# Performance work log

Hardware: AMD Instinct MI355X
Metric: run time of the kernel (lower is better)

The kernel has to match this reference:

```python
import jax, jax.numpy as jnp
import numpy as np

B, C, U, V, H, W = 4, 64, 5, 5, 64, 64
MID = 64  # mid_dim defaults to dim


def setup_inputs() -> dict:
    key = jax.random.key(0)
    ks = jax.random.split(key, 13)
    s = 0.05
    inp = {"x": jax.random.normal(ks[0], (B, C, U, V, H, W), dtype=jnp.float32)}
    # body: Conv2d(dim->mid,1x1), SiLU, Conv2d(mid->dim,1x1)
    inp["w1"] = jax.random.normal(ks[1], (MID, C), dtype=jnp.float32) * s
    inp["b1"] = jax.random.normal(ks[2], (MID,), dtype=jnp.float32) * s
    inp["w2"] = jax.random.normal(ks[3], (C, MID), dtype=jnp.float32) * s
    inp["b2"] = jax.random.normal(ks[4], (C,), dtype=jnp.float32) * s
    # four fuse 1x1 convs (dim->dim)
    for i in range(4):
        inp[f"fw{i}"] = jax.random.normal(ks[5 + 2 * i], (C, C), dtype=jnp.float32) * s
        inp[f"fb{i}"] = jax.random.normal(ks[6 + 2 * i], (C,), dtype=jnp.float32) * s
    return inp


def _conv1x1(w, b, x):
    # x: (B,C,h,w); w: (O,C); 1x1 conv == channel matmul
    return jnp.einsum('oc,bchw->bohw', w, x) + b[None, :, None, None]


def reference(x, w1, b1, w2, b2, fw0, fb0, fw1, fb1, fw2, fb2, fw3, fb3):
    # Four 2-axis mean pools over the 6D tensor
    hw_m = x.mean(axis=(2, 3))   # (B,C,H,W)
    uv_m = x.mean(axis=(4, 5))   # (B,C,U,V)
    uh_m = x.mean(axis=(3, 5))   # (B,C,U,H)
    vw_m = x.mean(axis=(2, 4))   # (B,C,V,W)
    # Assemble padded buffer uvhw of shape (B,C,H+V,W+U)
    top = jnp.concatenate([hw_m, jnp.swapaxes(uh_m, -1, -2)], axis=-1)  # (B,C,H,W+U)
    bot = jnp.concatenate([vw_m, jnp.swapaxes(uv_m, -1, -2)], axis=-1)  # (B,C,V,W+U)
    uvhw = jnpp_concat = jnp.concatenate([top, bot], axis=-2)           # (B,C,H+V,W+U)
    # body: conv1x1 -> SiLU -> conv1x1
    uvhw = _conv1x1(w2, b2, jax.nn.silu(_conv1x1(w1, b1, uvhw)))
    # Split back into the four pooled maps
    hw = uvhw[..., :H, :W]
    vw = uvhw[..., H:, :W]
    uh = jnp.swapaxes(uvhw[..., :H, W:], -1, -2)  # (B,C,U,H)
    uv = jnp.swapaxes(uvhw[..., H:, W:], -1, -2)  # (B,C,U,V)
    # Per-branch fuse convs, then broadcast-gate x and sum
    hw = _conv1x1(fw0, fb0, hw).reshape(B, C, 1, 1, H, W)
    uv = _conv1x1(fw1, fb1, uv).reshape(B, C, U, V, 1, 1)
    uh = _conv1x1(fw2, fb2, uh).reshape(B, C, U, 1, H, 1)
    vw = _conv1x1(fw3, fb3, vw).reshape(B, C, 1, V, 1, W)
    return x * hw + x * uv + x * uh + x * vw
```

## Files before the change

### kernel.cpp

```cpp
#include <hip/hip_runtime.h>
#include <hip/hip_bf16.h>
#include <cstddef>

#define BB 4
#define CC 64
#define UU 5
#define VV 5
#define HH 64
#define WW 64
#define NIJ (69*69)

typedef float f4v __attribute__((ext_vector_type(4)));

__device__ __forceinline__ float rdlane(float v, int l) {
    return __uint_as_float((unsigned)__builtin_amdgcn_readlane((int)__float_as_uint(v), l));
}
__device__ __forceinline__ float sum4(float4 a) { return (a.x+a.y)+(a.z+a.w); }
__device__ __forceinline__ void nt_store4(float4 r, float4* p) {
    union { float4 s; f4v v; } u; u.s = r;
    __builtin_nontemporal_store(u.v, (f4v*)p);
}

__global__ __launch_bounds__(512) void k1_means(const float* __restrict__ x,
        float* __restrict__ part_hw, float* __restrict__ part_vw,
        float* __restrict__ part_uv) {
    const int blk = blockIdx.x;
    const int bc  = blk / 5;
    const int u   = blk % 5;
    const int b   = bc >> 6;
    const int c   = bc & 63;
    const int pidx = (b*5 + u)*64 + c;
    const float4* xt = (const float4*)x + (size_t)bc * 25600 + (size_t)u * 5120;
    const int t    = threadIdx.x;
    const int wave = t >> 6;
    const int lane = t & 63;

    __shared__ float4 vw_lds[8][5][16];

    float4 A[5], B[5];
    #pragma unroll
    for (int v = 0; v < 5; ++v) {
        A[v] = xt[v*1024 + t];
        B[v] = xt[v*1024 + 512 + t];
    }

    float4 hw0 = make_float4(0.f,0.f,0.f,0.f);
    float4 hw1 = make_float4(0.f,0.f,0.f,0.f);
    float4 cs[5];
    #pragma unroll
    for (int v = 0; v < 5; ++v) {
        float4 a = A[v], d = B[v];
        hw0.x += a.x; hw0.y += a.y; hw0.z += a.z; hw0.w += a.w;
        hw1.x += d.x; hw1.y += d.y; hw1.z += d.z; hw1.w += d.w;
        cs[v].x = a.x + d.x; cs[v].y = a.y + d.y;
        cs[v].z = a.z + d.z; cs[v].w = a.w + d.w;
    }

    float4* ph4 = (float4*)part_hw + (size_t)pidx * 1024;
    ph4[t]       = hw0;
    ph4[512 + t] = hw1;

    #pragma unroll
    for (int v = 0; v < 5; ++v) {
        float4 s = cs[v];
        s.x += __shfl_xor(s.x, 16); s.y += __shfl_xor(s.y, 16);
        s.z += __shfl_xor(s.z, 16); s.w += __shfl_xor(s.w, 16);
        s.x += __shfl_xor(s.x, 32); s.y += __shfl_xor(s.y, 32);
        s.z += __shfl_xor(s.z, 32); s.w += __shfl_xor(s.w, 32);
        if (lane < 16) vw_lds[wave][v][lane] = s;
    }
    __syncthreads();

    if (t < 80) {
        const int v = t >> 4;
        float4 s = vw_lds[0][v][t & 15];
        #pragma unroll
        for (int w8 = 1; w8 < 8; ++w8) {
            float4 p = vw_lds[w8][v][t & 15];
            s.x += p.x; s.y += p.y; s.z += p.z; s.w += p.w;
        }
        ((float4*)part_vw)[(size_t)pidx*80 + t] = s;
        float hs = sum4(s);
        hs += __shfl_xor(hs, 1); hs += __shfl_xor(hs, 2);
        hs += __shfl_xor(hs, 4); hs += __shfl_xor(hs, 8);
        if ((t & 15) == 0)
            part_uv[((size_t)(b*5 + v)*5 + u)*64 + c] = hs;
    }
}

__global__ __launch_bounds__(512) void k1b_assemble(
        const float* __restrict__ part_hw, const float* __restrict__ part_vw,
        const float* __restrict__ part_uv, float* __restrict__ grid_t) {
    __shared__ float tile[64][68];
    const int blk = blockIdx.x;
    const bool top = blk < 256;
    const int t = threadIdx.x;
    const int c = t >> 3;
    const int q = t & 7;

    int b, i;
    if (top) {
        b = blk >> 6;
        const int h = blk & 63;
        i = h;
        float4 acc0 = make_float4(0.f,0.f,0.f,0.f);
        float4 acc1 = make_float4(0.f,0.f,0.f,0.f);
        float uhv[5];
        #pragma unroll
        for (int u = 0; u < 5; ++u) {
            const float4* src = (const float4*)part_hw
                + ((size_t)((b*5 + u)*64 + c)) * 1024 + h*16;
            float4 p0 = src[q];
            float4 p1 = src[8 + q];
            acc0.x += p0.x; acc0.y += p0.y; acc0.z += p0.z; acc0.w += p0.w;
            acc1.x += p1.x; acc1.y += p1.y; acc1.z += p1.z; acc1.w += p1.w;
            float uu = sum4(p0) + sum4(p1);
            uu += __shfl_xor(uu, 1); uu += __shfl_xor(uu, 2); uu += __shfl_xor(uu, 4);
            uhv[u] = uu;
        }
        const float s25 = 1.f/25.f;
        const int w0 = q*4, w1 = 32 + q*4;
        tile[w0+0][c] = acc0.x*s25; tile[w0+1][c] = acc0.y*s25;
        tile[w0+2][c] = acc0.z*s25; tile[w0+3][c] = acc0.w*s25;
        tile[w1+0][c] = acc1.x*s25; tile[w1+1][c] = acc1.y*s25;
        tile[w1+2][c] = acc1.z*s25; tile[w1+3][c] = acc1.w*s25;
        if (q == 0) {
            #pragma unroll
            for (int u = 0; u < 5; ++u)
                grid_t[((size_t)b*NIJ + h*69 + 64 + u)*64 + c] = uhv[u] * (1.f/320.f);
        }
    } else {
        b = (blk - 256) / 5;
        const int v = (blk - 256) % 5;
        i = 64 + v;
        float4 a0 = make_float4(0.f,0.f,0.f,0.f);
        float4 a1 = make_float4(0.f,0.f,0.f,0.f);
        #pragma unroll
        for (int u = 0; u < 5; ++u) {
            const float4* src = (const float4*)part_vw
                + ((size_t)((b*5 + u)*64 + c)) * 80 + v*16;
            float4 p0 = src[q];
            float4 p1 = src[8 + q];
            a0.x += p0.x; a0.y += p0.y; a0.z += p0.z; a0.w += p0.w;
            a1.x += p1.x; a1.y += p1.y; a1.z += p1.z; a1.w += p1.w;
        }
        const float sc = 1.f/320.f;
        const int w0 = q*4, w1 = 32 + q*4;
        tile[w0+0][c] = a0.x*sc; tile[w0+1][c] = a0.y*sc;
        tile[w0+2][c] = a0.z*sc; tile[w0+3][c] = a0.w*sc;
        tile[w1+0][c] = a1.x*sc; tile[w1+1][c] = a1.y*sc;
        tile[w1+2][c] = a1.z*sc; tile[w1+3][c] = a1.w*sc;
        if (t < 320) {
            const int u = t >> 6, cc = t & 63;
            grid_t[((size_t)b*NIJ + i*69 + 64 + u)*64 + cc] =
                part_uv[((size_t)(b*5 + v)*5 + u)*64 + cc] * (1.f/4096.f);
        }
    }
    __syncthreads();

    float4* dst4 = (float4*)grid_t + ((size_t)b*NIJ + i*69) * 16;
    #pragma unroll
    for (int k = 0; k < 2; ++k) {
        const int oidx = k*512 + t;
        const int w = oidx >> 4, cq = (oidx & 15) * 4;
        float4 v;
        v.x = tile[w][cq]; v.y = tile[w][cq+1];
        v.z = tile[w][cq+2]; v.w = tile[w][cq+3];
        dst4[oidx] = v;
    }
}

#define LOADROW(dst, src)                                              \
    { _Pragma("unroll")                                                \
      for (int q = 0; q < 16; ++q) {                                   \
          float4 t4 = ((const float4*)(src))[lane*16 + q];             \
          dst[4*q+0] = t4.x; dst[4*q+1] = t4.y;                        \
          dst[4*q+2] = t4.z; dst[4*q+3] = t4.w;                        \
      } }

#define DOT64(res, wr, src)                                            \
    float res;                                                         \
    { float _a0=0.f,_a1=0.f,_a2=0.f,_a3=0.f;                           \
      _Pragma("unroll")                                                \
      for (int cc2 = 0; cc2 < 64; cc2 += 4) {                          \
          _a0 = fmaf(wr[cc2+0], rdlane(src, cc2+0), _a0);              \
          _a1 = fmaf(wr[cc2+1], rdlane(src, cc2+1), _a1);              \
          _a2 = fmaf(wr[cc2+2], rdlane(src, cc2+2), _a2);              \
          _a3 = fmaf(wr[cc2+3], rdlane(src, cc2+3), _a3);              \
      }                                                                \
      res = (_a0 + _a1) + (_a2 + _a3); }

#define MLP_BODY(J)                                                    \
    {                                                                  \
        const int jj = (J);                                            \
        float v = gtb[(size_t)(i*69 + jj) * CC + lane];                \
        DOT64(d1, w1r, v);                                             \
        float acc1 = d1 + b1v;                                         \
        float ya = acc1 / (1.f + __expf(-acc1));                       \
        DOT64(d2, w2r, ya);                                            \
        float acc2 = d2 + b2v;                                         \
        DOT64(d3, fr, acc2);                                           \
        sp[(size_t)(jj - jbase) * sstr] = d3 + fbv;                    \
    }

__global__ __launch_bounds__(64, 1) void k2_mlp(
        const float* __restrict__ grid_t,
        const float* __restrict__ w1, const float* __restrict__ b1,
        const float* __restrict__ w2, const float* __restrict__ b2,
        const float* __restrict__ fw0, const float* __restrict__ fb0,
        const float* __restrict__ fw1, const float* __restrict__ fb1,
        const float* __restrict__ fw2, const float* __restrict__ fb2,
        const float* __restrict__ fw3, const float* __restrict__ fb3,
        float* __restrict__ mod_hw, float* __restrict__ mod_uh,
        float* __restrict__ mod_vw, float* __restrict__ mod_uv) {
    const int blk  = blockIdx.x;
    const int row  = blk >> 2;
    const int chnk = blk & 3;
    const int b    = row / 69;
    const int i    = row % 69;
    const int lane = threadIdx.x & 63;

    const int j0 = chnk * 18;
    const int j1 = min(69, j0 + 18);
    const bool top = (i < 64);

    const float* fwA = top ? fw0 : fw3;
    const float* fbA = top ? fb0 : fb3;
    const float* fwB = top ? fw2 : fw1;
    const float* fbB = top ? fb2 : fb1;

    float w1r[64], w2r[64], fr[64];
    LOADROW(w1r, w1);
    LOADROW(w2r, w2);
    const float b1v = b1[lane];
    const float b2v = b2[lane];

    const float* gtb = grid_t + (size_t)b * NIJ * CC;
    const int cbl = b * CC + lane;

    const int jm = min(j1, 64);
    if (j0 < jm) {
        LOADROW(fr, fwA);
        const float fbv = fbA[lane];
        float* sp; int sstr; const int jbase = 0;
        if (top) { sp = mod_hw + ((size_t)cbl*64 + i)*64;          sstr = 1; }
        else     { sp = mod_vw + (size_t)cbl*320 + (i-64)*64;      sstr = 1; }
        for (int j = j0; j < jm; ++j) MLP_BODY(j)
    }
    if (j1 > 64) {
        LOADROW(fr, fwB);
        const float fbv = fbB[lane];
        float* sp; int sstr; const int jbase = 64;
        if (top) { sp = mod_uh + (size_t)cbl*320 + i;              sstr = 64; }
        else     { sp = mod_uv + (size_t)cbl*25 + (i-64);          sstr = 5;  }
        const int jb = max(j0, 64);
        for (int j = jb; j < j1; ++j) MLP_BODY(j)
    }
}

__global__ __launch_bounds__(256) void k3_apply(
        const float* __restrict__ x,
        const float* __restrict__ mod_hw, const float* __restrict__ mod_uh,
        const float* __restrict__ mod_vw, const float* __restrict__ mod_uv,
        float* __restrict__ out) {
    const int blk  = blockIdx.x;
    const int bc   = blk >> 2;
    const int qt   = blk & 3;
    const int t    = threadIdx.x;
    const int base = qt*256 + t;
    const int h    = base >> 4;

    float4 mh = ((const float4*)(mod_hw + (size_t)bc * 4096))[base];
    float uh[5];
    #pragma unroll
    for (int u = 0; u < 5; ++u) uh[u] = mod_uh[(size_t)bc*320 + u*64 + h];
    float4 vw[5];
    #pragma unroll
    for (int v = 0; v < 5; ++v)
        vw[v] = ((const float4*)(mod_vw + (size_t)bc*320 + v*64))[t & 15];
    float uv[25];
    #pragma unroll
    for (int k = 0; k < 25; ++k) uv[k] = mod_uv[(size_t)bc*25 + k];

    const float4* x4 = (const float4*)(x + (size_t)bc * (UU*VV*HH*WW));
    float4* o4 = (float4*)(out + (size_t)bc * (UU*VV*HH*WW));

    #pragma unroll
    for (int u = 0; u < 5; ++u) {
        #pragma unroll
        for (int v = 0; v < 5; ++v) {
            const int idx = (u*5 + v)*1024 + base;
            float4 xv = x4[idx];
            const float s = uh[u] + uv[u*5 + v];
            float4 r;
            r.x = xv.x * (mh.x + vw[v].x + s);
            r.y = xv.y * (mh.y + vw[v].y + s);
            r.z = xv.z * (mh.z + vw[v].z + s);
            r.w = xv.w * (mh.w + vw[v].w + s);
            nt_store4(r, &o4[idx]);
        }
    }
}

extern "C" void kernel_launch(void* const* d_in, const int* in_sizes, int n_in,
                              void* d_out, int out_size, void* d_ws, size_t ws_size,
                              hipStream_t stream) {
    const float* x   = (const float*)d_in[0];
    const float* w1  = (const float*)d_in[1];
    const float* b1  = (const float*)d_in[2];
    const float* w2  = (const float*)d_in[3];
    const float* b2  = (const float*)d_in[4];
    const float* fw0 = (const float*)d_in[5];
    const float* fb0 = (const float*)d_in[6];
    const float* fw1 = (const float*)d_in[7];
    const float* fb1 = (const float*)d_in[8];
    const float* fw2 = (const float*)d_in[9];
    const float* fb2 = (const float*)d_in[10];
    const float* fw3 = (const float*)d_in[11];
    const float* fb3 = (const float*)d_in[12];

    float* ws = (float*)d_ws;
    float* grid_t = ws;
    float* mod_hw = ws + 1218816;
    float* mod_uh = mod_hw + 1048576;
    float* mod_vw = mod_uh + 81920;
    float* mod_uv = mod_vw + 81920;

    float* part_hw = (float*)d_out;
    float* part_vw = part_hw + 5242880;
    float* part_uv = part_vw + 409600;

    k1_means<<<BB*CC*UU, 512, 0, stream>>>(x, part_hw, part_vw, part_uv);
    k1b_assemble<<<BB*CC + BB*VV, 512, 0, stream>>>(part_hw, part_vw, part_uv, grid_t);
    k2_mlp<<<BB*69*4, 64, 0, stream>>>(grid_t, w1, b1, w2, b2,
                                       fw0, fb0, fw1, fb1, fw2, fb2, fw3, fb3,
                                       mod_hw, mod_uh, mod_vw, mod_uv);
    k3_apply<<<BB*CC*4, 256, 0, stream>>>(x, mod_hw, mod_uh, mod_vw, mod_uv,
                                          (float*)d_out);
}
```

Baseline: 108.4 us.

## Repartition mean reduction over (b,c,spatial-quarter) to shrink partial buffers

The first pass now assigns each block to one (b,c) and a quarter of the HW plane, looping over all 25 (u,v) slices. This lets it write final hw and uh means directly instead of per-u partials of the full HW plane, which were about 5x larger and had to be re-read by the assemble kernel. vw and uv still go through small per-quarter partials reduced in the assemble kernel. It also adds occupancy hints and readfirstlane for the uv scalars in the apply kernel. In exchange, each thread holds more registers (25 uv accumulators) and makes more cross-lane shuffles.

```diff
diff --git a/kernel.cpp b/kernel.cpp
--- a/kernel.cpp
+++ b/kernel.cpp
@@ -15,153 +15,160 @@
 __device__ __forceinline__ float rdlane(float v, int l) {
     return __uint_as_float((unsigned)__builtin_amdgcn_readlane((int)__float_as_uint(v), l));
 }
+__device__ __forceinline__ float rfl(float v) {
+    return __uint_as_float((unsigned)__builtin_amdgcn_readfirstlane((int)__float_as_uint(v)));
+}
 __device__ __forceinline__ float sum4(float4 a) { return (a.x+a.y)+(a.z+a.w); }
 __device__ __forceinline__ void nt_store4(float4 r, float4* p) {
     union { float4 s; f4v v; } u; u.s = r;
     __builtin_nontemporal_store(u.v, (f4v*)p);
 }
 
-__global__ __launch_bounds__(512) void k1_means(const float* __restrict__ x,
-        float* __restrict__ part_hw, float* __restrict__ part_vw,
-        float* __restrict__ part_uv) {
-    const int blk = blockIdx.x;
-    const int bc  = blk / 5;
-    const int u   = blk % 5;
-    const int b   = bc >> 6;
-    const int c   = bc & 63;
-    const int pidx = (b*5 + u)*64 + c;
-    const float4* xt = (const float4*)x + (size_t)bc * 25600 + (size_t)u * 5120;
-    const int t    = threadIdx.x;
+__global__ __launch_bounds__(256, 4) void k1_means(const float* __restrict__ x,
+        float* __restrict__ m_hw, float* __restrict__ m_uh,
+        float* __restrict__ vw_part, float* __restrict__ uv_part) {
+    const int bid = blockIdx.x;
+    const int bc  = bid >> 2;
+    const int qt  = bid & 3;
+    const int t   = threadIdx.x;
+    const int p   = qt*256 + t;
     const int wave = t >> 6;
     const int lane = t & 63;
 
-    __shared__ float4 vw_lds[8][5][16];
-
-    float4 A[5], B[5];
+    const float4* xt = (const float4*)x + (size_t)bc * 25600;
+
+    __shared__ float4 vw_lds[4][5][16];
+    __shared__ float  uv_lds[4][25];
+
+    float4 hw = make_float4(0.f,0.f,0.f,0.f);
+    float4 vwacc[5];
+    #pragma unroll
+    for (int v = 0; v < 5; ++v) vwacc[v] = make_float4(0.f,0.f,0.f,0.f);
+    float uvacc[25];
+
+    #pragma unroll
+    for (int u = 0; u < 5; ++u) {
+        float uhrow = 0.f;
+        #pragma unroll
+        for (int v = 0; v < 5; ++v) {
+            float4 q = xt[(u*5 + v)*1024 + p];
+            hw.x += q.x; hw.y += q.y; hw.z += q.z; hw.w += q.w;
+            vwacc[v].x += q.x; vwacc[v].y += q.y;
+            vwacc[v].z += q.z; vwacc[v].w += q.w;
+            float s4 = sum4(q);
+            uvacc[u*5 + v] = s4;
+            uhrow += s4;
+        }
+        float r = uhrow;
+        r += __shfl_xor(r, 1); r += __shfl_xor(r, 2);
+        r += __shfl_xor(r, 4); r += __shfl_xor(r, 8);
+        if ((t & 15) == 0)
+            m_uh[(size_t)bc*320 + u*64 + qt*16 + (t >> 4)] = r * (1.f/320.f);
+    }
+
+    float4 o;
+    o.x = hw.x*(1.f/25.f); o.y = hw.y*(1.f/25.f);
+    o.z = hw.z*(1.f/25.f); o.w = hw.w*(1.f/25.f);
+    ((float4*)m_hw)[(size_t)bc*1024 + p] = o;
+
     #pragma unroll
     for (int v = 0; v < 5; ++v) {
-        A[v] = xt[v*1024 + t];
-        B[v] = xt[v*1024 + 512 + t];
-    }
-
-    float4 hw0 = make_float4(0.f,0.f,0.f,0.f);
-    float4 hw1 = make_float4(0.f,0.f,0.f,0.f);
-    float4 cs[5];
-    #pragma unroll
-    for (int v = 0; v < 5; ++v) {
-        float4 a = A[v], d = B[v];
-        hw0.x += a.x; hw0.y += a.y; hw0.z += a.z; hw0.w += a.w;
-        hw1.x += d.x; hw1.y += d.y; hw1.z += d.z; hw1.w += d.w;
-        cs[v].x = a.x + d.x; cs[v].y = a.y + d.y;
-        cs[v].z = a.z + d.z; cs[v].w = a.w + d.w;
-    }
-
-    float4* ph4 = (float4*)part_hw + (size_t)pidx * 1024;
-    ph4[t]       = hw0;
-    ph4[512 + t] = hw1;
-
-    #pragma unroll
-    for (int v = 0; v < 5; ++v) {
-        float4 s = cs[v];
+        float4 s = vwacc[v];
         s.x += __shfl_xor(s.x, 16); s.y += __shfl_xor(s.y, 16);
         s.z += __shfl_xor(s.z, 16); s.w += __shfl_xor(s.w, 16);
         s.x += __shfl_xor(s.x, 32); s.y += __shfl_xor(s.y, 32);
         s.z += __shfl_xor(s.z, 32); s.w += __shfl_xor(s.w, 32);
         if (lane < 16) vw_lds[wave][v][lane] = s;
     }
+    #pragma unroll
+    for (int k = 0; k < 25; ++k) {
+        float s = uvacc[k];
+        s += __shfl_xor(s, 1); s += __shfl_xor(s, 2);
+        s += __shfl_xor(s, 4); s += __shfl_xor(s, 8);
+        s += __shfl_xor(s, 16); s += __shfl_xor(s, 32);
+        if (lane == 0) uv_lds[wave][k] = s;
+    }
     __syncthreads();
 
     if (t < 80) {
         const int v = t >> 4;
         float4 s = vw_lds[0][v][t & 15];
         #pragma unroll
-        for (int w8 = 1; w8 < 8; ++w8) {
-            float4 p = vw_lds[w8][v][t & 15];
-            s.x += p.x; s.y += p.y; s.z += p.z; s.w += p.w;
-        }
-        ((float4*)part_vw)[(size_t)pidx*80 + t] = s;
-        float hs = sum4(s);
-        hs += __shfl_xor(hs, 1); hs += __shfl_xor(hs, 2);
-        hs += __shfl_xor(hs, 4); hs += __shfl_xor(hs, 8);
-        if ((t & 15) == 0)
-            part_uv[((size_t)(b*5 + v)*5 + u)*64 + c] = hs;
-    }
-}
-
-__global__ __launch_bounds__(512) void k1b_assemble(
-        const float* __restrict__ part_hw, const float* __restrict__ part_vw,
-        const float* __restrict__ part_uv, float* __restrict__ grid_t) {
+        for (int w4 = 1; w4 < 4; ++w4) {
+            float4 pp = vw_lds[w4][v][t & 15];
+            s.x += pp.x; s.y += pp.y; s.z += pp.z; s.w += pp.w;
+        }
+        ((float4*)vw_part)[(size_t)bid*80 + t] = s;
+    }
+    if (t < 25) {
+        float s = uv_lds[0][t] + uv_lds[1][t] + uv_lds[2][t] + uv_lds[3][t];
+        uv_part[(size_t)bid*25 + t] = s;
+    }
+}
+
+__global__ __launch_bounds__(256) void k1b_assemble(
+        const float* __restrict__ m_hw, const float* __restrict__ m_uh,
+        const float* __restrict__ vw_part, const float* __restrict__ uv_part,
+        float* __restrict__ grid_t) {
     __shared__ float tile[64][68];
     const int blk = blockIdx.x;
     const bool top = blk < 256;
     const int t = threadIdx.x;
-    const int c = t >> 3;
-    const int q = t & 7;
+    const int c = t >> 2;
+    const int qs = t & 3;
 
     int b, i;
     if (top) {
         b = blk >> 6;
         const int h = blk & 63;
         i = h;
-        float4 acc0 = make_float4(0.f,0.f,0.f,0.f);
-        float4 acc1 = make_float4(0.f,0.f,0.f,0.f);
-        float uhv[5];
-        #pragma unroll
-        for (int u = 0; u < 5; ++u) {
-            const float4* src = (const float4*)part_hw
-                + ((size_t)((b*5 + u)*64 + c)) * 1024 + h*16;
-            float4 p0 = src[q];
-            float4 p1 = src[8 + q];
-            acc0.x += p0.x; acc0.y += p0.y; acc0.z += p0.z; acc0.w += p0.w;
-            acc1.x += p1.x; acc1.y += p1.y; acc1.z += p1.z; acc1.w += p1.w;
-            float uu = sum4(p0) + sum4(p1);
-            uu += __shfl_xor(uu, 1); uu += __shfl_xor(uu, 2); uu += __shfl_xor(uu, 4);
-            uhv[u] = uu;
-        }
-        const float s25 = 1.f/25.f;
-        const int w0 = q*4, w1 = 32 + q*4;
-        tile[w0+0][c] = acc0.x*s25; tile[w0+1][c] = acc0.y*s25;
-        tile[w0+2][c] = acc0.z*s25; tile[w0+3][c] = acc0.w*s25;
-        tile[w1+0][c] = acc1.x*s25; tile[w1+1][c] = acc1.y*s25;
-        tile[w1+2][c] = acc1.z*s25; tile[w1+3][c] = acc1.w*s25;
-        if (q == 0) {
-            #pragma unroll
-            for (int u = 0; u < 5; ++u)
-                grid_t[((size_t)b*NIJ + h*69 + 64 + u)*64 + c] = uhv[u] * (1.f/320.f);
+        #pragma unroll
+        for (int j = 0; j < 4; ++j) {
+            const int q = 4*j + qs;
+            float4 v = ((const float4*)m_hw)[((size_t)(b*64 + c))*1024 + h*16 + q];
+            const int w = q * 4;
+            tile[w+0][c] = v.x; tile[w+1][c] = v.y;
+            tile[w+2][c] = v.z; tile[w+3][c] = v.w;
+        }
+        for (int idx = t; idx < 320; idx += 256) {
+            const int u = idx >> 6, cc = idx & 63;
+            grid_t[((size_t)b*NIJ + h*69 + 64 + u)*64 + cc] =
+                m_uh[(size_t)(b*64 + cc)*320 + u*64 + h];
         }
     } else {
         b = (blk - 256) / 5;
         const int v = (blk - 256) % 5;
         i = 64 + v;
-        float4 a0 = make_float4(0.f,0.f,0.f,0.f);
-        float4 a1 = make_float4(0.f,0.f,0.f,0.f);
-        #pragma unroll
-        for (int u = 0; u < 5; ++u) {
-            const float4* src = (const float4*)part_vw
-                + ((size_t)((b*5 + u)*64 + c)) * 80 + v*16;
-            float4 p0 = src[q];
-            float4 p1 = src[8 + q];
-            a0.x += p0.x; a0.y += p0.y; a0.z += p0.z; a0.w += p0.w;
-            a1.x += p1.x; a1.y += p1.y; a1.z += p1.z; a1.w += p1.w;
-        }
-        const float sc = 1.f/320.f;
-        const int w0 = q*4, w1 = 32 + q*4;
-        tile[w0+0][c] = a0.x*sc; tile[w0+1][c] = a0.y*sc;
-        tile[w0+2][c] = a0.z*sc; tile[w0+3][c] = a0.w*sc;
-        tile[w1+0][c] = a1.x*sc; tile[w1+1][c] = a1.y*sc;
-        tile[w1+2][c] = a1.z*sc; tile[w1+3][c] = a1.w*sc;
-        if (t < 320) {
-            const int u = t >> 6, cc = t & 63;
-            grid_t[((size_t)b*NIJ + i*69 + 64 + u)*64 + cc] =
-                part_uv[((size_t)(b*5 + v)*5 + u)*64 + cc] * (1.f/4096.f);
+        #pragma unroll
+        for (int j = 0; j < 4; ++j) {
+            const int wq = 4*j + qs;
+            float4 acc = make_float4(0.f,0.f,0.f,0.f);
+            #pragma unroll
+            for (int qt = 0; qt < 4; ++qt) {
+                float4 p = ((const float4*)vw_part)
+                    [((size_t)(b*64 + c)*4 + qt)*80 + v*16 + wq];
+                acc.x += p.x; acc.y += p.y; acc.z += p.z; acc.w += p.w;
+            }
+            const int w = wq * 4;
+            const float sc = 1.f/320.f;
+            tile[w+0][c] = acc.x*sc; tile[w+1][c] = acc.y*sc;
+            tile[w+2][c] = acc.z*sc; tile[w+3][c] = acc.w*sc;
+        }
+        for (int idx = t; idx < 320; idx += 256) {
+            const int u = idx >> 6, cc = idx & 63;
+            float s = 0.f;
+            #pragma unroll
+            for (int qt = 0; qt < 4; ++qt)
+                s += uv_part[((size_t)(b*64 + cc)*4 + qt)*25 + u*5 + v];
+            grid_t[((size_t)b*NIJ + i*69 + 64 + u)*64 + cc] = s * (1.f/4096.f);
         }
     }
     __syncthreads();
 
     float4* dst4 = (float4*)grid_t + ((size_t)b*NIJ + i*69) * 16;
     #pragma unroll
-    for (int k = 0; k < 2; ++k) {
-        const int oidx = k*512 + t;
+    for (int k = 0; k < 4; ++k) {
+        const int oidx = k*256 + t;
         const int w = oidx >> 4, cq = (oidx & 15) * 4;
         float4 v;
         v.x = tile[w][cq]; v.y = tile[w][cq+1];
@@ -258,7 +265,7 @@
     }
 }
 
-__global__ __launch_bounds__(256) void k3_apply(
+__global__ __launch_bounds__(256, 4) void k3_apply(
         const float* __restrict__ x,
         const float* __restrict__ mod_hw, const float* __restrict__ mod_uh,
         const float* __restrict__ mod_vw, const float* __restrict__ mod_uv,
@@ -280,7 +287,8 @@
         vw[v] = ((const float4*)(mod_vw + (size_t)bc*320 + v*64))[t & 15];
     float uv[25];
     #pragma unroll
-    for (int k = 0; k < 25; ++k) uv[k] = mod_uv[(size_t)bc*25 + k];
+    for (int k = 0; k < 25; ++k)
+        uv[k] = rfl(mod_uv[(size_t)bc*25 + k]);
 
     const float4* x4 = (const float4*)(x + (size_t)bc * (UU*VV*HH*WW));
     float4* o4 = (float4*)(out + (size_t)bc * (UU*VV*HH*WW));
@@ -326,12 +334,13 @@
     float* mod_vw = mod_uh + 81920;
     float* mod_uv = mod_vw + 81920;
 
-    float* part_hw = (float*)d_out;
-    float* part_vw = part_hw + 5242880;
-    float* part_uv = part_vw + 409600;
-
-    k1_means<<<BB*CC*UU, 512, 0, stream>>>(x, part_hw, part_vw, part_uv);
-    k1b_assemble<<<BB*CC + BB*VV, 512, 0, stream>>>(part_hw, part_vw, part_uv, grid_t);
+    float* m_hw    = (float*)d_out;
+    float* m_uh    = m_hw + 1048576;
+    float* vw_part = m_uh + 81920;
+    float* uv_part = vw_part + 327680;
+
+    k1_means<<<BB*CC*4, 256, 0, stream>>>(x, m_hw, m_uh, vw_part, uv_part);
+    k1b_assemble<<<BB*CC + BB*VV, 256, 0, stream>>>(m_hw, m_uh, vw_part, uv_part, grid_t);
     k2_mlp<<<BB*69*4, 64, 0, stream>>>(grid_t, w1, b1, w2, b2,
                                        fw0, fb0, fw1, fb1, fw2, fb2, fw3, fb3,
                                        mod_hw, mod_uh, mod_vw, mod_uv);
```

Result: slower. 115.6 us (+6.6%).
